# Performance work log

Hardware: AMD Instinct MI355X
Metric: run time of the kernel (lower is better)

Reference implementation:

```python
import jax, jax.numpy as jnp
import numpy as np

NUM_HEADS = 8
D_HEAD = 64
LN_EPS = 1e-6


def _pad_idx(lengths, max_len):
    # flat indices into a [B*max_len, ...] dense buffer for each packed token
    return np.concatenate([b * max_len + np.arange(int(l)) for b, l in enumerate(lengths)])


def _layer_norm(x, scale, bias):
    mu = jnp.mean(x, axis=-1, keepdims=True)
    var = jnp.mean(jnp.square(x - mu), axis=-1, keepdims=True)
    return (x - mu) * jax.lax.rsqrt(var + LN_EPS) * scale + bias


def setup_inputs() -> dict:
    key = jax.random.key(0)
    ks = jax.random.split(key, 12)
    d_model, d_ff, H, dh = 512, 2048, NUM_HEADS, D_HEAD
    lengths = np.array([128 * (i + 1) for i in range(8)], dtype=np.int64)  # sum = 4608
    total = int(lengths.sum())
    s = 0.02
    return {
        "x": jax.random.normal(ks[0], (total, d_model), jnp.float32),
        "mem": jax.random.normal(ks[1], (total, d_model), jnp.float32),
        "lengths_x": lengths,
        "lengths_mem": lengths.copy(),
        "Wq": jax.random.normal(ks[2], (d_model, H * dh), jnp.float32) * s,
        "Wk": jax.random.normal(ks[3], (d_model, H * dh), jnp.float32) * s,
        "Wv": jax.random.normal(ks[4], (d_model, H * dh), jnp.float32) * s,
        "Wo": jax.random.normal(ks[5], (H * dh, d_model), jnp.float32) * s,
        "ln1_scale": jnp.ones((d_model,), jnp.float32),
        "ln1_bias": jnp.zeros((d_model,), jnp.float32),
        "W1": jax.random.normal(ks[6], (d_model, d_ff), jnp.float32) * s,
        "b1": jnp.zeros((d_ff,), jnp.float32),
        "W2": jax.random.normal(ks[7], (d_ff, d_model), jnp.float32) * s,
        "b2": jnp.zeros((d_model,), jnp.float32),
        "ln2_scale": jnp.ones((d_model,), jnp.float32),
        "ln2_bias": jnp.zeros((d_model,), jnp.float32),
    }


def reference(x, mem, lengths_x, lengths_mem, Wq, Wk, Wv, Wo,
              ln1_scale, ln1_bias, W1, b1, W2, b2, ln2_scale, ln2_bias):
    lx = np.asarray(lengths_x)
    lm = np.asarray(lengths_mem)
    B = lx.shape[0]
    Lx = int(lx.max())
    Lm = int(lm.max())
    H, dh = NUM_HEADS, D_HEAD

    idx_x = _pad_idx(lx, Lx)
    idx_m = _pad_idx(lm, Lm)

    def pad(packed, idx, B, L):
        dense = jnp.zeros((B * L,) + packed.shape[1:], packed.dtype).at[idx].set(packed)
        return dense.reshape((B, L) + packed.shape[1:])

    q = pad((x @ Wq).reshape(-1, H, dh), idx_x, B, Lx)   # [B, Lx, H, dh]
    k = pad((mem @ Wk).reshape(-1, H, dh), idx_m, B, Lm)  # [B, Lm, H, dh]
    v = pad((mem @ Wv).reshape(-1, H, dh), idx_m, B, Lm)

    e = jnp.einsum('bxhd,byhd->bhxy', q, k) / np.sqrt(dh)  # [B, H, Lx, Lm]
    # validity mask: (query pos < len_x) & (key pos < len_mem)
    mask = (np.arange(Lx)[None, :, None] < lx[:, None, None]) & \
           (np.arange(Lm)[None, None, :] < lm[:, None, None])
    mask = jnp.asarray(mask)[:, None, :, :]  # [B, 1, Lx, Lm]
    e = jnp.where(mask, e, jnp.float32(-1e30))  # finite -inf surrogate; identical softmax on valid rows
    alpha = jax.nn.softmax(e, axis=-1)
    out = jnp.einsum('bhxy,byhd->bxhd', alpha, v).reshape(B, Lx, H * dh)
    out = out @ Wo                                  # [B, Lx, d_model]
    out = out.reshape(B * Lx, -1)[idx_x]            # pack back to [total_x, d_model]

    h = _layer_norm(x + out, ln1_scale, ln1_bias)
    ffn = jax.nn.relu(h @ W1 + b1) @ W2 + b2
    return _layer_norm(h + ffn, ln2_scale, ln2_bias)
```

## Files before the change

### kernel.cpp

```cpp
#include <hip/hip_runtime.h>
#include <stdint.h>

typedef short bf8v __attribute__((ext_vector_type(8)));
typedef float f4v  __attribute__((ext_vector_type(4)));
typedef short s8v  __attribute__((ext_vector_type(8)));

__device__ __forceinline__ float bf2f(short b){
  unsigned u = ((unsigned)(unsigned short)b) << 16;
  union { unsigned u; float f; } c; c.u = u; return c.f;
}
__device__ __forceinline__ short f2bf(float f){
  union { float f; unsigned u; } c; c.f = f;
  unsigned r = (c.u + 0x7FFFu + ((c.u >> 16) & 1u)) >> 16;
  return (short)r;
}
__device__ __forceinline__ void gload16(const short* g, short* l){
  __builtin_amdgcn_global_load_lds(
      (const __attribute__((address_space(1))) void*)g,
      (__attribute__((address_space(3))) void*)l, 16, 0, 0);
}

__global__ void prep_kernel(const int* lx, const int* lm, int* meta){
  if (threadIdx.x != 0) return;
  int is64 = ((lx[1] | lx[3] | lx[5] | lx[7]) == 0) ? 1 : 0;
  int ox = 0, om = 0;
  for (int b = 0; b < 8; ++b){
    int a = is64 ? lx[2*b] : lx[b];
    int c = is64 ? lm[2*b] : lm[b];
    meta[b] = a; meta[8+b] = c;
    meta[16+b] = ox; meta[25+b] = om;
    ox += a; om += c;
  }
  meta[24] = ox; meta[33] = om;
}

__global__ __launch_bounds__(256) void cvt2bf(const float* __restrict__ x,
                                              const float* __restrict__ mem,
                                              short* __restrict__ xb,
                                              short* __restrict__ mb,
                                              long long n){
  long long t = (long long)blockIdx.x * 256 + threadIdx.x;
  long long i = t * 8;
  const float* s; short* d;
  if (i < n){ s = x + i; d = xb + i; }
  else {
    i -= n; if (i >= n) return;
    s = mem + i; d = mb + i;
  }
  float4 f0 = *(const float4*)s;
  float4 f1 = *(const float4*)(s + 4);
  s8v o;
  o[0]=f2bf(f0.x); o[1]=f2bf(f0.y); o[2]=f2bf(f0.z); o[3]=f2bf(f0.w);
  o[4]=f2bf(f1.x); o[5]=f2bf(f1.y); o[6]=f2bf(f1.z); o[7]=f2bf(f1.w);
  *(s8v*)d = o;
}

__global__ __launch_bounds__(256) void cvt_w_t(
    const float* __restrict__ Wq, const float* __restrict__ Wk,
    const float* __restrict__ Wv, const float* __restrict__ Wo,
    const float* __restrict__ W1, const float* __restrict__ W2,
    short* __restrict__ WqT, short* __restrict__ WkT,
    short* __restrict__ WvT, short* __restrict__ WoT,
    short* __restrict__ W1T, short* __restrict__ W2T){
  __shared__ float tile[32][33];
  int bid = blockIdx.x;
  const float* W; short* WT; int K, N, t0;
  if      (bid <  256){ W=Wq; WT=WqT; K=512;  N=512;  t0=0;    }
  else if (bid <  512){ W=Wk; WT=WkT; K=512;  N=512;  t0=256;  }
  else if (bid <  768){ W=Wv; WT=WvT; K=512;  N=512;  t0=512;  }
  else if (bid < 1024){ W=Wo; WT=WoT; K=512;  N=512;  t0=768;  }
  else if (bid < 2048){ W=W1; WT=W1T; K=512;  N=2048; t0=1024; }
  else                { W=W2; WT=W2T; K=2048; N=512;  t0=2048; }
  int lt = bid - t0;
  int ntn = N / 32;
  int tk = lt / ntn, tn = lt % ntn;
  int r0 = threadIdx.x >> 5, c = threadIdx.x & 31;
  #pragma unroll
  for (int i = 0; i < 4; ++i){
    int r = r0 + i*8;
    tile[r][c] = W[(long)(tk*32 + r)*N + tn*32 + c];
  }
  __syncthreads();
  #pragma unroll
  for (int i = 0; i < 4; ++i){
    int r = r0 + i*8;
    WT[(long)(tn*32 + r)*K + tk*32 + c] = f2bf(tile[c][r]);
  }
}

__device__ __forceinline__ void stage_gemm(const short* A, const short* Bt,
    long brow, long bcol, int M, int N, int K, int t,
    short* Als, short* Bls){
  int tid = threadIdx.x;
  #pragma unroll
  for (int i = 0; i < 2; ++i){
    int c = i*256 + tid;
    int row = c >> 2, slot = c & 3;
    int cg = slot ^ ((row >> 1) & 3);
    long ar = brow + row; if (ar >= M) ar = M - 1;
    gload16(A + ar*(long)K + t + cg*8, &Als[c*8]);
    long br = bcol + row; if (br >= N) br = N - 1;
    gload16(Bt + br*(long)K + t + cg*8, &Bls[c*8]);
  }
}

__device__ __forceinline__ void gemm_core(const short* A, const short* Bt,
    short* __restrict__ C, const float* __restrict__ bias,
    int M, int N, int K, float scale, int relu, int colmajor,
    long brow, long bcol, short* Als, short* Bls){
  int tid = threadIdx.x;
  int lane = tid & 63, w = tid >> 6;
  int wm = w >> 1, wn = w & 1;
  int l15 = lane & 15, l4 = lane >> 4;

  f4v acc[4][4];
  #pragma unroll
  for (int m = 0; m < 4; ++m)
    #pragma unroll
    for (int n = 0; n < 4; ++n) acc[m][n] = (f4v){0.f,0.f,0.f,0.f};

  int nt = K / 32;
  stage_gemm(A, Bt, brow, bcol, M, N, K, 0, Als, Bls);
  for (int t = 0; t < nt; ++t){
    __syncthreads();
    if (t + 1 < nt)
      stage_gemm(A, Bt, brow, bcol, M, N, K, (t+1)*32,
                 Als + ((t+1)&1)*4096, Bls + ((t+1)&1)*4096);
    const short* Ab = Als + (t&1)*4096;
    const short* Bb = Bls + (t&1)*4096;
    bf8v a[4], b[4];
    #pragma unroll
    for (int m = 0; m < 4; ++m){
      int row = wm*64 + m*16 + l15;
      int slot = l4 ^ ((row >> 1) & 3);
      a[m] = *(const bf8v*)&Ab[row*32 + slot*8];
    }
    #pragma unroll
    for (int n = 0; n < 4; ++n){
      int row = wn*64 + n*16 + l15;
      int slot = l4 ^ ((row >> 1) & 3);
      b[n] = *(const bf8v*)&Bb[row*32 + slot*8];
    }
    #pragma unroll
    for (int m = 0; m < 4; ++m)
      #pragma unroll
      for (int n = 0; n < 4; ++n)
        acc[m][n] = __builtin_amdgcn_mfma_f32_16x16x32_bf16(a[m], b[n], acc[m][n], 0, 0, 0);
  }

  #pragma unroll
  for (int m = 0; m < 4; ++m){
    #pragma unroll
    for (int n = 0; n < 4; ++n){
      long col = bcol + wn*64 + n*16 + l15;
      float bi = (bias != nullptr && col < N) ? bias[col] : 0.f;
      #pragma unroll
      for (int j = 0; j < 4; ++j){
        long row = brow + wm*64 + m*16 + 4*l4 + j;
        if (row < M && col < N){
          float v = acc[m][n][j] * scale + bi;
          if (relu) v = fmaxf(v, 0.f);
          C[colmajor ? (col*(long)M + row) : (row*(long)N + col)] = f2bf(v);
        }
      }
    }
  }
}

__global__ __launch_bounds__(256) void gemm_bt(
    const short* __restrict__ A, const short* __restrict__ Bt,
    short* __restrict__ C, const float* __restrict__ bias,
    int M, int N, int K, float scale, int relu, int colmajor){
  __shared__ __align__(16) short Als[2*128*32];
  __shared__ __align__(16) short Bls[2*128*32];
  gemm_core(A, Bt, C, bias, M, N, K, scale, relu, colmajor,
            (long)blockIdx.y * 128, (long)blockIdx.x * 128, Als, Bls);
}

__global__ __launch_bounds__(256) void gemm_qkv(
    const short* __restrict__ xb, const short* __restrict__ mb,
    const short* __restrict__ WqT, const short* __restrict__ WkT,
    const short* __restrict__ WvT,
    short* __restrict__ Qb, short* __restrict__ Kbf, short* __restrict__ Vtb,
    int total){
  __shared__ __align__(16) short Als[2*128*32];
  __shared__ __align__(16) short Bls[2*128*32];
  int seg = blockIdx.x >> 2;
  const short* A  = (seg == 0) ? xb : mb;
  const short* Bt = (seg == 0) ? WqT : ((seg == 1) ? WkT : WvT);
  short* C        = (seg == 0) ? Qb  : ((seg == 1) ? Kbf : Vtb);
  float scale     = (seg == 0) ? 0.125f : 1.f;
  int colmajor    = (seg == 2);
  gemm_core(A, Bt, C, nullptr, total, 512, 512, scale, 0, colmajor,
            (long)blockIdx.y * 128, (long)(blockIdx.x & 3) * 128, Als, Bls);
}

__global__ __launch_bounds__(512) void attn_kernel(
    const short* __restrict__ Q, const short* __restrict__ Kb,
    const short* __restrict__ Vt, short* __restrict__ Ob,
    const int* __restrict__ meta, int total){
  int qt = blockIdx.x, h = blockIdx.y, b = blockIdx.z;
  int Lx = meta[b], Lm = meta[8+b];
  int ox = meta[16+b], om = meta[25+b];
  if (qt*128 >= Lx) return;

  __shared__ __align__(16) short Kls[2][64*64];
  __shared__ __align__(16) short Vls[2][64*64];
  __shared__ __align__(16) short Pls[8][16*64];

  int tid = threadIdx.x;
  int lane = tid & 63, w = tid >> 6;
  int l15 = lane & 15, l4 = lane >> 4;

  bf8v aq0, aq1;
  {
    int qrow = qt*128 + w*16 + l15;
    int grow = ox + (qrow < Lx ? qrow : Lx - 1);
    const short* qp = Q + (long)grow*512 + h*64 + l4*8;
    aq0 = *(const bf8v*)qp;
    aq1 = *(const bf8v*)(qp + 32);
  }
  float mrun[4] = {-1e30f,-1e30f,-1e30f,-1e30f};
  float lrun[4] = {0.f,0.f,0.f,0.f};
  f4v o[4];
  #pragma unroll
  for (int n = 0; n < 4; ++n) o[n] = (f4v){0.f,0.f,0.f,0.f};

  int nt = (Lm + 63) / 64;

  #define ATTN_STAGE(T, BUF)                                                   \
    {                                                                          \
      int c = tid;                                                             \
      int rr = c >> 3, slot = c & 7;                                           \
      int ch = slot ^ (rr & 7);                                                \
      int kv0_ = (T) * 64;                                                     \
      int tok = kv0_ + rr; if (tok >= Lm) tok = Lm - 1;                        \
      gload16(Kb + (long)(om + tok)*512 + h*64 + ch*8, &Kls[BUF][c*8]);        \
      int kvs = kv0_ + ch*8; if (kvs + 8 > Lm) kvs = Lm - 8;                   \
      gload16(Vt + (long)(h*64 + rr)*total + om + kvs, &Vls[BUF][c*8]);        \
    }

  ATTN_STAGE(0, 0)
  for (int t = 0; t < nt; ++t){
    __syncthreads();
    if (t + 1 < nt) ATTN_STAGE(t+1, (t+1)&1)
    int buf = t & 1;
    int kv0 = t * 64;

    f4v s[4];
    #pragma unroll
    for (int n = 0; n < 4; ++n){
      int kvrow = n*16 + l15;
      int sl0 = l4 ^ (kvrow & 7);
      int sl1 = (4 + l4) ^ (kvrow & 7);
      bf8v b0 = *(const bf8v*)&Kls[buf][kvrow*64 + sl0*8];
      bf8v b1 = *(const bf8v*)&Kls[buf][kvrow*64 + sl1*8];
      f4v z = (f4v){0.f,0.f,0.f,0.f};
      z = __builtin_amdgcn_mfma_f32_16x16x32_bf16(aq0, b0, z, 0, 0, 0);
      z = __builtin_amdgcn_mfma_f32_16x16x32_bf16(aq1, b1, z, 0, 0, 0);
      s[n] = z;
    }
    #pragma unroll
    for (int n = 0; n < 4; ++n){
      if (kv0 + n*16 + l15 >= Lm){
        s[n][0] = -1e30f; s[n][1] = -1e30f; s[n][2] = -1e30f; s[n][3] = -1e30f;
      }
    }
    #pragma unroll
    for (int j = 0; j < 4; ++j){
      float m1 = fmaxf(fmaxf(s[0][j], s[1][j]), fmaxf(s[2][j], s[3][j]));
      m1 = fmaxf(m1, __shfl_xor(m1, 1, 64));
      m1 = fmaxf(m1, __shfl_xor(m1, 2, 64));
      m1 = fmaxf(m1, __shfl_xor(m1, 4, 64));
      m1 = fmaxf(m1, __shfl_xor(m1, 8, 64));
      float mnew = fmaxf(mrun[j], m1);
      float sc = __expf(mrun[j] - mnew);
      float rs = 0.f;
      #pragma unroll
      for (int n = 0; n < 4; ++n){
        float p = __expf(s[n][j] - mnew);
        s[n][j] = p; rs += p;
      }
      rs += __shfl_xor(rs, 1, 64); rs += __shfl_xor(rs, 2, 64);
      rs += __shfl_xor(rs, 4, 64); rs += __shfl_xor(rs, 8, 64);
      lrun[j] = lrun[j] * sc + rs;
      mrun[j] = mnew;
      o[0][j] *= sc; o[1][j] *= sc; o[2][j] *= sc; o[3][j] *= sc;
    }
    #pragma unroll
    for (int n = 0; n < 4; ++n){
      int pcol = n*16 + l15;
      #pragma unroll
      for (int j = 0; j < 4; ++j){
        int prow = 4*l4 + j;
        Pls[w][prow*64 + (((pcol >> 3) ^ (prow & 7)) << 3) + (pcol & 7)] = f2bf(s[n][j]);
      }
    }
    #pragma unroll
    for (int ks = 0; ks < 2; ++ks){
      int ch = ks*4 + l4;
      bf8v ap = *(const bf8v*)&Pls[w][l15*64 + ((ch ^ (l15 & 7)) << 3)];
      #pragma unroll
      for (int n = 0; n < 4; ++n){
        int d = n*16 + l15;
        bf8v bv = *(const bf8v*)&Vls[buf][d*64 + ((ch ^ (d & 7)) << 3)];
        o[n] = __builtin_amdgcn_mfma_f32_16x16x32_bf16(ap, bv, o[n], 0, 0, 0);
      }
    }
  }
  #undef ATTN_STAGE

  #pragma unroll
  for (int n = 0; n < 4; ++n){
    #pragma unroll
    for (int j = 0; j < 4; ++j){
      int qrow = qt*128 + w*16 + 4*l4 + j;
      if (qrow < Lx){
        float val = o[n][j] / lrun[j];
        Ob[(long)(ox + qrow)*512 + h*64 + n*16 + l15] = f2bf(val);
      }
    }
  }
}

__global__ __launch_bounds__(256) void ln_fuse(
    const float* __restrict__ Af, const short* __restrict__ Ab,
    const short* __restrict__ Bb,
    const float* __restrict__ gamma, const float* __restrict__ beta,
    short* __restrict__ outb, float* __restrict__ outf, int rows){
  int w = threadIdx.x >> 6, lane = threadIdx.x & 63;
  long row = (long)blockIdx.x * 4 + w;
  if (row >= rows) return;
  int c0 = lane * 8;
  long base = row * 512 + c0;
  float v[8];
  if (Af){
    float4 f0 = *(const float4*)(Af + base);
    float4 f1 = *(const float4*)(Af + base + 4);
    v[0]=f0.x; v[1]=f0.y; v[2]=f0.z; v[3]=f0.w;
    v[4]=f1.x; v[5]=f1.y; v[6]=f1.z; v[7]=f1.w;
  } else {
    s8v a = *(const s8v*)(Ab + base);
    #pragma unroll
    for (int j = 0; j < 8; ++j) v[j] = bf2f(a[j]);
  }
  s8v bb = *(const s8v*)(Bb + base);
  #pragma unroll
  for (int j = 0; j < 8; ++j) v[j] += bf2f(bb[j]);
  float sum = 0.f;
  #pragma unroll
  for (int j = 0; j < 8; ++j) sum += v[j];
  #pragma unroll
  for (int m = 1; m < 64; m <<= 1) sum += __shfl_xor(sum, m, 64);
  float mu = sum * (1.f/512.f);
  float q = 0.f;
  #pragma unroll
  for (int j = 0; j < 8; ++j){ float d = v[j] - mu; q += d*d; }
  #pragma unroll
  for (int m = 1; m < 64; m <<= 1) q += __shfl_xor(q, m, 64);
  float rs = rsqrtf(q * (1.f/512.f) + 1e-6f);
  float ov[8];
  #pragma unroll
  for (int j = 0; j < 8; ++j)
    ov[j] = (v[j] - mu) * rs * gamma[c0 + j] + beta[c0 + j];
  if (outb){
    s8v os;
    #pragma unroll
    for (int j = 0; j < 8; ++j) os[j] = f2bf(ov[j]);
    *(s8v*)(outb + base) = os;
  } else {
    float4 f0 = {ov[0], ov[1], ov[2], ov[3]};
    float4 f1 = {ov[4], ov[5], ov[6], ov[7]};
    *(float4*)(outf + base) = f0;
    *(float4*)(outf + base + 4) = f1;
  }
}

extern "C" void kernel_launch(void* const* d_in, const int* in_sizes, int n_in,
                              void* d_out, int out_size, void* d_ws, size_t ws_size,
                              hipStream_t stream){
  (void)n_in; (void)out_size; (void)ws_size;
  const float* x   = (const float*)d_in[0];
  const float* mem = (const float*)d_in[1];
  const int*   lxr = (const int*)d_in[2];
  const int*   lmr = (const int*)d_in[3];
  const float* Wq  = (const float*)d_in[4];
  const float* Wk  = (const float*)d_in[5];
  const float* Wv  = (const float*)d_in[6];
  const float* Wo  = (const float*)d_in[7];
  const float* g1  = (const float*)d_in[8];
  const float* be1 = (const float*)d_in[9];
  const float* W1  = (const float*)d_in[10];
  const float* b1  = (const float*)d_in[11];
  const float* W2  = (const float*)d_in[12];
  const float* b2  = (const float*)d_in[13];
  const float* g2  = (const float*)d_in[14];
  const float* be2 = (const float*)d_in[15];
  float* out = (float*)d_out;

  int total = in_sizes[0] / 512;
  if (total <= 0) return;
  long long n = (long long)total * 512;

  char* p = (char*)d_ws;
  int*   meta = (int*)p;    p += 256;
  short* xb   = (short*)p;  p += n*2;
  short* mb   = (short*)p;  p += n*2;
  short* Qb   = (short*)p;  p += n*2;
  short* Kbf  = (short*)p;  p += n*2;
  short* Vtb  = (short*)p;  p += n*2;
  short* attnb= (short*)p;  p += n*2;
  short* woout= (short*)p;  p += n*2;
  short* hb   = (short*)p;  p += n*2;
  short* ffn1 = (short*)p;  p += (long long)total*2048*2;
  short* ffn2 = (short*)p;  p += n*2;
  short* WqT  = (short*)p;  p += 512*512*2;
  short* WkT  = (short*)p;  p += 512*512*2;
  short* WvT  = (short*)p;  p += 512*512*2;
  short* WoT  = (short*)p;  p += 512*512*2;
  short* W1T  = (short*)p;  p += 2048*512*2;
  short* W2T  = (short*)p;  p += 512*2048*2;

  prep_kernel<<<1, 64, 0, stream>>>(lxr, lmr, meta);

  long long th = (2*n)/8;
  cvt2bf<<<dim3((unsigned)((th + 255)/256)), dim3(256), 0, stream>>>(x, mem, xb, mb, n);
  cvt_w_t<<<dim3(3072), dim3(256), 0, stream>>>(Wq,Wk,Wv,Wo,W1,W2, WqT,WkT,WvT,WoT,W1T,W2T);

  int mt = (total + 127)/128;
  gemm_qkv<<<dim3(12, mt), 256, 0, stream>>>(xb, mb, WqT, WkT, WvT, Qb, Kbf, Vtb, total);

  attn_kernel<<<dim3((unsigned)((total + 127)/128), 8, 8), 512, 0, stream>>>(Qb, Kbf, Vtb, attnb, meta, total);

  gemm_bt<<<dim3(4, mt), 256, 0, stream>>>(attnb, WoT, woout, nullptr, total, 512, 512, 1.f, 0, 0);
  ln_fuse<<<dim3((unsigned)((total + 3)/4)), 256, 0, stream>>>(x, nullptr, woout, g1, be1, hb, nullptr, total);

  gemm_bt<<<dim3(16, mt), 256, 0, stream>>>(hb,   W1T, ffn1, b1, total, 2048, 512,  1.f, 1, 0);
  gemm_bt<<<dim3(4,  mt), 256, 0, stream>>>(ffn1, W2T, ffn2, b2, total, 512,  2048, 1.f, 0, 0);
  ln_fuse<<<dim3((unsigned)((total + 3)/4)), 256, 0, stream>>>(nullptr, hb, ffn2, g2, be2, nullptr, out, total);
}
```

Measured before the change: 204.5 us.

## Use 64-row GEMM tiles for narrow GEMMs and triple-buffer attention KV loads

Result: faster. 184.4 us (-9.8%).

```diff
diff --git a/kernel.cpp b/kernel.cpp
--- a/kernel.cpp
+++ b/kernel.cpp
@@ -88,75 +88,85 @@
   }
 }
 
+template<int BM>
 __device__ __forceinline__ void stage_gemm(const short* A, const short* Bt,
     long brow, long bcol, int M, int N, int K, int t,
     short* Als, short* Bls){
   int tid = threadIdx.x;
   #pragma unroll
-  for (int i = 0; i < 2; ++i){
-    int c = i*256 + tid;
-    int row = c >> 2, slot = c & 3;
+  for (int i = 0; i < BM/64; ++i){
+    int cc = i*256 + tid;
+    int row = cc >> 2, slot = cc & 3;
     int cg = slot ^ ((row >> 1) & 3);
     long ar = brow + row; if (ar >= M) ar = M - 1;
-    gload16(A + ar*(long)K + t + cg*8, &Als[c*8]);
+    gload16(A + ar*(long)K + t + cg*8, &Als[cc*8]);
+  }
+  #pragma unroll
+  for (int i = 0; i < 2; ++i){
+    int cc = i*256 + tid;
+    int row = cc >> 2, slot = cc & 3;
+    int cg = slot ^ ((row >> 1) & 3);
     long br = bcol + row; if (br >= N) br = N - 1;
-    gload16(Bt + br*(long)K + t + cg*8, &Bls[c*8]);
-  }
-}
-
+    gload16(Bt + br*(long)K + t + cg*8, &Bls[cc*8]);
+  }
+}
+
+template<int BM>
 __device__ __forceinline__ void gemm_core(const short* A, const short* Bt,
     short* __restrict__ C, const float* __restrict__ bias,
     int M, int N, int K, float scale, int relu, int colmajor,
     long brow, long bcol, short* Als, short* Bls){
+  constexpr int NREP = (BM == 128) ? 4 : 2;
   int tid = threadIdx.x;
   int lane = tid & 63, w = tid >> 6;
-  int wm = w >> 1, wn = w & 1;
+  int wrow = (BM == 128) ? (w >> 1) * 64 : 0;
+  int wcol = (BM == 128) ? (w & 1) * 64 : w * 32;
   int l15 = lane & 15, l4 = lane >> 4;
 
-  f4v acc[4][4];
+  f4v acc[4][NREP];
   #pragma unroll
   for (int m = 0; m < 4; ++m)
     #pragma unroll
-    for (int n = 0; n < 4; ++n) acc[m][n] = (f4v){0.f,0.f,0.f,0.f};
+    for (int n = 0; n < NREP; ++n) acc[m][n] = (f4v){0.f,0.f,0.f,0.f};
 
   int nt = K / 32;
-  stage_gemm(A, Bt, brow, bcol, M, N, K, 0, Als, Bls);
+  stage_gemm<BM>(A, Bt, brow, bcol, M, N, K, 0, Als, Bls);
   for (int t = 0; t < nt; ++t){
     __syncthreads();
     if (t + 1 < nt)
-      stage_gemm(A, Bt, brow, bcol, M, N, K, (t+1)*32,
-                 Als + ((t+1)&1)*4096, Bls + ((t+1)&1)*4096);
-    const short* Ab = Als + (t&1)*4096;
+      stage_gemm<BM>(A, Bt, brow, bcol, M, N, K, (t+1)*32,
+                     Als + ((t+1)&1)*(BM*32), Bls + ((t+1)&1)*4096);
+    const short* Ab = Als + (t&1)*(BM*32);
     const short* Bb = Bls + (t&1)*4096;
-    bf8v a[4], b[4];
+    bf8v a[4], b[NREP];
     #pragma unroll
     for (int m = 0; m < 4; ++m){
-      int row = wm*64 + m*16 + l15;
+      int row = wrow + m*16 + l15;
       int slot = l4 ^ ((row >> 1) & 3);
       a[m] = *(const bf8v*)&Ab[row*32 + slot*8];
     }
     #pragma unroll
-    for (int n = 0; n < 4; ++n){
-      int row = wn*64 + n*16 + l15;
+    for (int n = 0; n < NREP; ++n){
+      int row = wcol + n*16 + l15;
       int slot = l4 ^ ((row >> 1) & 3);
       b[n] = *(const bf8v*)&Bb[row*32 + slot*8];
     }
     #pragma unroll
     for (int m = 0; m < 4; ++m)
       #pragma unroll
-      for (int n = 0; n < 4; ++n)
+      for (int n = 0; n < NREP; ++n)
         acc[m][n] = __builtin_amdgcn_mfma_f32_16x16x32_bf16(a[m], b[n], acc[m][n], 0, 0, 0);
   }
 
   #pragma unroll
   for (int m = 0; m < 4; ++m){
     #pragma unroll
-    for (int n = 0; n < 4; ++n){
-      long col = bcol + wn*64 + n*16 + l15;
+    for (int n = 0; n < NREP; ++n){
+      long col = bcol + wcol + n*16 + l15;
       float bi = (bias != nullptr && col < N) ? bias[col] : 0.f;
       #pragma unroll
       for (int j = 0; j < 4; ++j){
-        long row = brow + wm*64 + m*16 + 4*l4 + j;
+        long row = brow + wrow + m*16 + 4*l4 + j;
         if (row < M && col < N){
           float v = acc[m][n][j] * scale + bi;
           if (relu) v = fmaxf(v, 0.f);
@@ -173,8 +183,18 @@
     int M, int N, int K, float scale, int relu, int colmajor){
   __shared__ __align__(16) short Als[2*128*32];
   __shared__ __align__(16) short Bls[2*128*32];
-  gemm_core(A, Bt, C, bias, M, N, K, scale, relu, colmajor,
-            (long)blockIdx.y * 128, (long)blockIdx.x * 128, Als, Bls);
+  gemm_core<128>(A, Bt, C, bias, M, N, K, scale, relu, colmajor,
+                 (long)blockIdx.y * 128, (long)blockIdx.x * 128, Als, Bls);
+}
+
+__global__ __launch_bounds__(256) void gemm_bt64(
+    const short* __restrict__ A, const short* __restrict__ Bt,
+    short* __restrict__ C, const float* __restrict__ bias,
+    int M, int N, int K, float scale, int relu, int colmajor){
+  __shared__ __align__(16) short Als[2*64*32];
+  __shared__ __align__(16) short Bls[2*128*32];
+  gemm_core<64>(A, Bt, C, bias, M, N, K, scale, relu, colmajor,
+                (long)blockIdx.y * 64, (long)blockIdx.x * 128, Als, Bls);
 }
 
 __global__ __launch_bounds__(256) void gemm_qkv(
@@ -183,7 +203,7 @@
     const short* __restrict__ WvT,
     short* __restrict__ Qb, short* __restrict__ Kbf, short* __restrict__ Vtb,
     int total){
-  __shared__ __align__(16) short Als[2*128*32];
+  __shared__ __align__(16) short Als[2*64*32];
   __shared__ __align__(16) short Bls[2*128*32];
   int seg = blockIdx.x >> 2;
   const short* A  = (seg == 0) ? xb : mb;
@@ -191,8 +211,8 @@
   short* C        = (seg == 0) ? Qb  : ((seg == 1) ? Kbf : Vtb);
   float scale     = (seg == 0) ? 0.125f : 1.f;
   int colmajor    = (seg == 2);
-  gemm_core(A, Bt, C, nullptr, total, 512, 512, scale, 0, colmajor,
-            (long)blockIdx.y * 128, (long)(blockIdx.x & 3) * 128, Als, Bls);
+  gemm_core<64>(A, Bt, C, nullptr, total, 512, 512, scale, 0, colmajor,
+                (long)blockIdx.y * 64, (long)(blockIdx.x & 3) * 128, Als, Bls);
 }
 
 __global__ __launch_bounds__(512) void attn_kernel(
@@ -204,8 +224,8 @@
   int ox = meta[16+b], om = meta[25+b];
   if (qt*128 >= Lx) return;
 
-  __shared__ __align__(16) short Kls[2][64*64];
-  __shared__ __align__(16) short Vls[2][64*64];
+  __shared__ __align__(16) short Kls[3][64*64];
+  __shared__ __align__(16) short Vls[3][64*64];
   __shared__ __align__(16) short Pls[8][16*64];
 
   int tid = threadIdx.x;
@@ -241,10 +261,18 @@
     }
 
   ATTN_STAGE(0, 0)
+  if (1 < nt) ATTN_STAGE(1, 1)
+
+  int buf = 0;
   for (int t = 0; t < nt; ++t){
-    __syncthreads();
-    if (t + 1 < nt) ATTN_STAGE(t+1, (t+1)&1)
-    int buf = t & 1;
+    if (t + 1 < nt) asm volatile("s_waitcnt vmcnt(2)" ::: "memory");
+    else            asm volatile("s_waitcnt vmcnt(0)" ::: "memory");
+    __builtin_amdgcn_s_barrier();
+    asm volatile("" ::: "memory");
+    if (t + 2 < nt){
+      int bs = buf + 2; if (bs >= 3) bs -= 3;
+      ATTN_STAGE(t+2, bs)
+    }
     int kv0 = t * 64;
 
     f4v s[4];
@@ -307,6 +335,7 @@
         o[n] = __builtin_amdgcn_mfma_f32_16x16x32_bf16(ap, bv, o[n], 0, 0, 0);
       }
     }
+    buf = (buf + 1 == 3) ? 0 : buf + 1;
   }
   #undef ATTN_STAGE
 
@@ -427,15 +456,16 @@
   cvt2bf<<<dim3((unsigned)((th + 255)/256)), dim3(256), 0, stream>>>(x, mem, xb, mb, n);
   cvt_w_t<<<dim3(3072), dim3(256), 0, stream>>>(Wq,Wk,Wv,Wo,W1,W2, WqT,WkT,WvT,WoT,W1T,W2T);
 
-  int mt = (total + 127)/128;
-  gemm_qkv<<<dim3(12, mt), 256, 0, stream>>>(xb, mb, WqT, WkT, WvT, Qb, Kbf, Vtb, total);
+  int mt128 = (total + 127)/128;
+  int mt64  = (total + 63)/64;
+  gemm_qkv<<<dim3(12, mt64), 256, 0, stream>>>(xb, mb, WqT, WkT, WvT, Qb, Kbf, Vtb, total);
 
   attn_kernel<<<dim3((unsigned)((total + 127)/128), 8, 8), 512, 0, stream>>>(Qb, Kbf, Vtb, attnb, meta, total);
 
-  gemm_bt<<<dim3(4, mt), 256, 0, stream>>>(attnb, WoT, woout, nullptr, total, 512, 512, 1.f, 0, 0);
+  gemm_bt64<<<dim3(4, mt64), 256, 0, stream>>>(attnb, WoT, woout, nullptr, total, 512, 512, 1.f, 0, 0);
   ln_fuse<<<dim3((unsigned)((total + 3)/4)), 256, 0, stream>>>(x, nullptr, woout, g1, be1, hb, nullptr, total);
 
-  gemm_bt<<<dim3(16, mt), 256, 0, stream>>>(hb,   W1T, ffn1, b1, total, 2048, 512,  1.f, 1, 0);
-  gemm_bt<<<dim3(4,  mt), 256, 0, stream>>>(ffn1, W2T, ffn2, b2, total, 512,  2048, 1.f, 0, 0);
+  gemm_bt<<<dim3(16, mt128), 256, 0, stream>>>(hb,   W1T, ffn1, b1, total, 2048, 512,  1.f, 1, 0);
+  gemm_bt64<<<dim3(4, mt64), 256, 0, stream>>>(ffn1, W2T, ffn2, b2, total, 512,  2048, 1.f, 0, 0);
   ln_fuse<<<dim3((unsigned)((total + 3)/4)), 256, 0, stream>>>(nullptr, hb, ffn2, g2, be2, nullptr, out, total);
 }
```
